# Optimization experiments

Hardware: AMD Instinct MI355X
Metric: run time of the kernel (lower is better)

## Reference

```python
import jax, jax.numpy as jnp
import numpy as np

EPS = 1e-6
NUM_HEADS = 16

def _rmsnorm(h, w):
    hf = h.astype(jnp.float32)
    var = jnp.mean(hf * hf, axis=-1, keepdims=True)
    return (w * (hf * jax.lax.rsqrt(var + EPS))).astype(h.dtype)

def _rotary(t, cos, sin):
    # t: [B,N,H,hd]; cos/sin: [N, hd//2]
    tf = t.astype(jnp.float32)
    tr = tf[..., 0::2]
    ti = tf[..., 1::2]
    c = cos[None, :, None, :]
    s = sin[None, :, None, :]
    out_r = tr * c - ti * s
    out_i = tr * s + ti * c
    out = jnp.stack([out_r, out_i], axis=-1).reshape(t.shape)
    return out.astype(t.dtype)

def setup_inputs() -> dict:
    key = jax.random.key(0)
    ks = jax.random.split(key, 8)
    B, N, C = 2, 2048, 1024
    hd = C // NUM_HEADS
    x = jax.random.normal(ks[0], (B, N, C), jnp.float32)
    qkv_w = jax.random.normal(ks[1], (3 * C, C), jnp.float32) * (C ** -0.5)
    q_norm_w = jnp.ones((hd,), jnp.float32)
    k_norm_w = jnp.ones((hd,), jnp.float32)
    proj_w = jax.random.normal(ks[2], (C, C), jnp.float32) * (C ** -0.5)
    proj_b = jnp.zeros((C,), jnp.float32)
    # rotary freqs_cis = exp(i * theta): unit-magnitude cos/sin
    inv_freq = 1.0 / (10000.0 ** (jnp.arange(0, hd, 2, dtype=jnp.float32) / hd))
    ang = jnp.arange(N, dtype=jnp.float32)[:, None] * inv_freq[None, :]
    pos_cos = jnp.cos(ang)
    pos_sin = jnp.sin(ang)
    mask = jnp.tril(jnp.ones((N, N), dtype=bool))
    return {"x": x, "qkv_w": qkv_w, "q_norm_w": q_norm_w, "k_norm_w": k_norm_w,
            "proj_w": proj_w, "proj_b": proj_b, "pos_cos": pos_cos,
            "pos_sin": pos_sin, "mask": mask}

def reference(x, qkv_w, q_norm_w, k_norm_w, proj_w, proj_b, pos_cos, pos_sin, mask):
    B, N, C = x.shape
    H = NUM_HEADS
    hd = C // H
    qkv = (x @ qkv_w.T).reshape(B, N, 3, H, hd)
    q, k, v = qkv[:, :, 0], qkv[:, :, 1], qkv[:, :, 2]  # [B,N,H,hd]
    q = _rmsnorm(q, q_norm_w)
    k = _rmsnorm(k, k_norm_w)
    q = _rotary(q, pos_cos, pos_sin)
    k = _rotary(k, pos_cos, pos_sin)
    q = q.transpose(0, 2, 1, 3)  # [B,H,N,hd]
    k = k.transpose(0, 2, 1, 3)
    v = v.transpose(0, 2, 1, 3)
    scale = hd ** -0.5
    scores = jnp.einsum('bhqd,bhkd->bhqk', q, k) * scale
    scores = jnp.where(mask[None, None, :, :], scores, jnp.float32(-1e30))
    attn = jax.nn.softmax(scores, axis=-1)
    out = jnp.einsum('bhqk,bhkd->bhqd', attn, v)
    out = out.transpose(0, 2, 1, 3).reshape(B, N, C)
    return out @ proj_w.T + proj_b
```

## Files before the change

kernel.cpp:

```cpp
#include <hip/hip_runtime.h>

using u16 = unsigned short;
using short4v = __attribute__((ext_vector_type(4))) short;
using short8 = __attribute__((ext_vector_type(8))) short;
using floatx4 = __attribute__((ext_vector_type(4))) float;

__device__ __forceinline__ float bf2f(u16 h) {
  union { unsigned int u; float f; } v;
  v.u = ((unsigned int)h) << 16;
  return v.f;
}
__device__ __forceinline__ u16 f2bf(float f) {
  union { float f; unsigned int u; } v;
  v.f = f;
  unsigned int u = v.u;
  return (u16)((u + 0x7FFFu + ((u >> 16) & 1u)) >> 16);
}
__device__ __forceinline__ u16 f2bf_rtz(float f) {
  union { float f; unsigned int u; } v;
  v.f = f;
  return (u16)(v.u >> 16);
}

__device__ __forceinline__ float exp2_raw(float x) {
  return __builtin_amdgcn_exp2f(x);
}
__device__ __forceinline__ float rcp_raw(float x) {
  return __builtin_amdgcn_rcpf(x);
}

typedef const __attribute__((address_space(1))) unsigned int* gas_t;
typedef __attribute__((address_space(3))) unsigned int* las_t;
__device__ __forceinline__ void gl_lds16(const u16* g, u16* l) {
  __builtin_amdgcn_global_load_lds((gas_t)(const void*)g, (las_t)(void*)l, 16,
                                   0, 0);
}

#define MFMA32 __builtin_amdgcn_mfma_f32_16x16x32_bf16

#define QSCALE 0.180336880111f

__global__ __launch_bounds__(256) void cvt_all(
    const float* __restrict__ x, const float* __restrict__ wq,
    const float* __restrict__ wp, u16* __restrict__ xb, u16* __restrict__ wqb,
    u16* __restrict__ wpb) {
#pragma unroll
  for (int j = 0; j < 4; j++) {
    int i = blockIdx.x * 256 + threadIdx.x + j * 524288;
    const float* src;
    u16* dst;
    int off;
    if (i < 1048576) {
      src = x; dst = xb; off = i;
    } else if (i < 1048576 + 786432) {
      src = wq; dst = wqb; off = i - 1048576;
    } else {
      src = wp; dst = wpb; off = i - 1835008;
    }
    float4 v = ((const float4*)src)[off];
    ushort4 o;
    o.x = f2bf(v.x);
    o.y = f2bf(v.y);
    o.z = f2bf(v.z);
    o.w = f2bf(v.w);
    ((ushort4*)dst)[off] = o;
  }
}

template <int BIAS, int OUTBF16, int MT>
__global__ __launch_bounds__(256) void gemm_nt(
    const u16* __restrict__ A, const u16* __restrict__ B,
    const float* __restrict__ bias, void* __restrict__ Cout,
    int M, int N, int K) {
  constexpr int ROWS_A = MT * 32;
  __shared__ u16 As[ROWS_A * 64];
  __shared__ u16 Bs[128 * 64];
  const int tid = threadIdx.x;
  const int lane = tid & 63;
  const int wave = tid >> 6;
  const int col = lane & 15;
  const int quad = lane >> 4;
  const int bm = blockIdx.y * ROWS_A;
  const int bn = blockIdx.x * 128;
  const int wm = (wave >> 1) * (MT * 16);
  const int wn = (wave & 1) * 64;
  const int rsw = col & 7;

  floatx4 acc[MT][4] = {};

  for (int kb = 0; kb < K; kb += 64) {
    __syncthreads();
#pragma unroll
    for (int c = tid; c < ROWS_A * 8; c += 256) {
      const int row = c >> 3, s = (c & 7) ^ (row & 7);
      gl_lds16(A + (size_t)(bm + row) * K + kb + s * 8, As + c * 8);
    }
#pragma unroll
    for (int c = tid; c < 1024; c += 256) {
      const int row = c >> 3, s = (c & 7) ^ (row & 7);
      gl_lds16(B + (size_t)(bn + row) * K + kb + s * 8, Bs + c * 8);
    }
    __syncthreads();

#pragma unroll
    for (int kk = 0; kk < 2; kk++) {
      short8 af[MT], bfr[4];
#pragma unroll
      for (int i = 0; i < MT; i++)
        af[i] = *(const short8*)(As + (wm + i * 16 + col) * 64 +
                                 ((kk * 4 + quad) ^ rsw) * 8);
#pragma unroll
      for (int i = 0; i < 4; i++)
        bfr[i] = *(const short8*)(Bs + (wn + i * 16 + col) * 64 +
                                  ((kk * 4 + quad) ^ rsw) * 8);
#pragma unroll
      for (int mi = 0; mi < MT; mi++)
#pragma unroll
        for (int ni = 0; ni < 4; ni++)
          acc[mi][ni] = MFMA32(af[mi], bfr[ni], acc[mi][ni], 0, 0, 0);
    }
  }

#pragma unroll
  for (int mi = 0; mi < MT; mi++) {
#pragma unroll
    for (int ni = 0; ni < 4; ni++) {
#pragma unroll
      for (int r = 0; r < 4; r++) {
        int row = bm + wm + mi * 16 + quad * 4 + r;
        int c = bn + wn + ni * 16 + col;
        float v = acc[mi][ni][r];
        if (BIAS) v += bias[c];
        if (OUTBF16)
          ((u16*)Cout)[(size_t)row * N + c] = f2bf(v);
        else
          ((float*)Cout)[(size_t)row * N + c] = v;
      }
    }
  }
}

__global__ __launch_bounds__(256) void gemm_qkv(
    const u16* __restrict__ A, const u16* __restrict__ B,
    const float* __restrict__ qw, const float* __restrict__ kw,
    const float* __restrict__ pcos, const float* __restrict__ psin,
    u16* __restrict__ Qb, u16* __restrict__ Kb, u16* __restrict__ Vt) {
  constexpr int K = 1024;
  __shared__ u16 As[128 * 64];
  __shared__ u16 Bs[128 * 64];
  const int tid = threadIdx.x;
  const int lane = tid & 63;
  const int wave = tid >> 6;
  const int col = lane & 15;
  const int quad = lane >> 4;
  const int bm = blockIdx.y * 128;
  const int bn = blockIdx.x * 128;
  const int wm = (wave >> 1) * 64;
  const int wn = (wave & 1) * 64;
  const int rsw = col & 7;

  floatx4 acc[4][4] = {};

  for (int kb = 0; kb < K; kb += 64) {
    __syncthreads();
#pragma unroll
    for (int c = tid; c < 1024; c += 256) {
      const int row = c >> 3, s = (c & 7) ^ (row & 7);
      gl_lds16(A + (size_t)(bm + row) * K + kb + s * 8, As + c * 8);
    }
#pragma unroll
    for (int c = tid; c < 1024; c += 256) {
      const int row = c >> 3, s = (c & 7) ^ (row & 7);
      gl_lds16(B + (size_t)(bn + row) * K + kb + s * 8, Bs + c * 8);
    }
    __syncthreads();

#pragma unroll
    for (int kk = 0; kk < 2; kk++) {
      short8 af[4], bfr[4];
#pragma unroll
      for (int i = 0; i < 4; i++)
        af[i] = *(const short8*)(As + (wm + i * 16 + col) * 64 +
                                 ((kk * 4 + quad) ^ rsw) * 8);
#pragma unroll
      for (int i = 0; i < 4; i++)
        bfr[i] = *(const short8*)(Bs + (wn + i * 16 + col) * 64 +
                                  ((kk * 4 + quad) ^ rsw) * 8);
#pragma unroll
      for (int mi = 0; mi < 4; mi++)
#pragma unroll
        for (int ni = 0; ni < 4; ni++)
          acc[mi][ni] = MFMA32(af[mi], bfr[ni], acc[mi][ni], 0, 0, 0);
    }
  }

  const int c0 = bn + wn;
  const int type = c0 >> 10;
  const int h = (c0 >> 6) & 15;
  const int b = bm >> 11;
  const int bh = b * 16 + h;
  const int nt0 = (bm & 2047) + wm;

  __syncthreads();

  if (type == 2) {
#pragma unroll
    for (int mi = 0; mi < 4; mi++) {
#pragma unroll
      for (int ni = 0; ni < 4; ni++) {
        const int d = ni * 16 + col;
        const int n0 = nt0 + mi * 16 + quad * 4;
        short4v pk;
#pragma unroll
        for (int r = 0; r < 4; r++) pk[r] = (short)f2bf(acc[mi][ni][r]);
        *(short4v*)&Vt[((size_t)(bh * 64 + d)) * 2048 + n0] = pk;
      }
    }
  } else {
    u16* const T = (wave < 2 ? As : Bs) + (wave & 1) * 4096;
    u16* const dst = type ? Kb : Qb;
    const float* const nw = type ? kw : qw;
    float wloc[4];
#pragma unroll
    for (int ni = 0; ni < 4; ni++) wloc[ni] = nw[ni * 16 + col];

#pragma unroll
    for (int mh = 0; mh < 2; mh++) {
#pragma unroll
      for (int mm = 0; mm < 2; mm++) {
        const int mi = mh * 2 + mm;
        floatx4 ss = {};
#pragma unroll
        for (int ni = 0; ni < 4; ni++)
#pragma unroll
          for (int r = 0; r < 4; r++)
            ss[r] += acc[mi][ni][r] * acc[mi][ni][r];
#pragma unroll
        for (int off = 1; off <= 8; off <<= 1)
#pragma unroll
          for (int r = 0; r < 4; r++) ss[r] += __shfl_xor(ss[r], off);
        floatx4 rn;
#pragma unroll
        for (int r = 0; r < 4; r++)
          rn[r] = rsqrtf(ss[r] * (1.0f / 64.0f) + 1e-6f);

#pragma unroll
        for (int ni = 0; ni < 4; ni++) {
          float nv[4], pv[4];
#pragma unroll
          for (int r = 0; r < 4; r++)
            nv[r] = acc[mi][ni][r] * rn[r] * wloc[ni];
#pragma unroll
          for (int r = 0; r < 4; r++) pv[r] = __shfl_xor(nv[r], 1);
#pragma unroll
          for (int r = 0; r < 4; r++) {
            const int n = nt0 + mi * 16 + quad * 4 + r;
            const float cc = pcos[n * 32 + ni * 8 + (col >> 1)];
            const float sn = psin[n * 32 + ni * 8 + (col >> 1)];
            float out = (col & 1) ? pv[r] * sn + nv[r] * cc
                                  : nv[r] * cc - pv[r] * sn;
            if (type == 0) out *= QSCALE;
            T[(mm * 16 + quad * 4 + r) * 80 + ni * 16 + col] = f2bf(out);
          }
        }
      }
      const int tl = lane >> 3;
      const int dc = (lane & 7) * 8;
#pragma unroll
      for (int i = 0; i < 4; i++) {
        short8 v = *(const short8*)&T[(i * 8 + tl) * 80 + dc];
        const int n = nt0 + mh * 32 + i * 8 + tl;
        *(short8*)&dst[((size_t)(bh * 2048 + n)) * 64 + dc] = v;
      }
    }
  }
}

__global__ __launch_bounds__(256) void attn_flash(
    const u16* __restrict__ Q, const u16* __restrict__ Kk,
    const u16* __restrict__ Vt, u16* __restrict__ O) {
  __shared__ u16 Ks[2][2][64 * 32];
  __shared__ u16 Vs[2][2][64 * 32];
  __shared__ u16 Pb[4][16 * 64];
  const int id = blockIdx.x;
  const int bh = id & 31;
  const int tile = 31 - (id >> 5);
  const int tid = threadIdx.x;
  const int lane = tid & 63;
  const int wave = tid >> 6;
  const int col = lane & 15;
  const int quad = lane >> 4;
  const int srow = tid >> 2;
  const int sswz = ((tid & 3) ^ (srow & 3)) * 8;
  const int rq = (quad ^ (col & 3)) * 8;
  const int pswz = (col & 7) << 1;

  const u16* Qh = Q + (size_t)bh * 2048 * 64;
  const u16* Kh = Kk + (size_t)bh * 2048 * 64;
  const u16* Vh = Vt + (size_t)bh * 64 * 2048;
  const int b = bh >> 4, h = bh & 15;

  const int q0 = tile * 64 + wave * 16;

  short8 aq[2];
#pragma unroll
  for (int ks = 0; ks < 2; ks++)
    aq[ks] = *(const short8*)(Qh + (size_t)(q0 + col) * 64 + ks * 32 + quad * 8);

  short8 ones;
#pragma unroll
  for (int j = 0; j < 8; j++) ones[j] = (short)0x3F80;

  floatx4 accO[4] = {};
  floatx4 lacc = {};
  const int nsteps = tile + 1;

#pragma unroll
  for (int half = 0; half < 2; half++) {
    gl_lds16(Kh + (size_t)srow * 64 + half * 32 + sswz,
             &Ks[0][half][0] + tid * 8);
    gl_lds16(Vh + (size_t)srow * 2048 + half * 32 + sswz,
             &Vs[0][half][0] + tid * 8);
  }
  __syncthreads();

  int cur = 0;
  for (int kt = 0; kt < nsteps; kt++) {
    const int j0 = kt * 64;

    if (kt + 1 < nsteps) {
      const int j1 = j0 + 64;
#pragma unroll
      for (int half = 0; half < 2; half++) {
        gl_lds16(Kh + (size_t)(j1 + srow) * 64 + half * 32 + sswz,
                 &Ks[cur ^ 1][half][0] + tid * 8);
        gl_lds16(Vh + (size_t)srow * 2048 + j1 + half * 32 + sswz,
                 &Vs[cur ^ 1][half][0] + tid * 8);
      }
    }

    floatx4 s[4] = {};
#pragma unroll
    for (int nt = 0; nt < 4; nt++) {
#pragma unroll
      for (int ks = 0; ks < 2; ks++) {
        short8 bk = *(const short8*)&Ks[cur][ks][(nt * 16 + col) * 32 + rq];
        s[nt] = MFMA32(bk, aq[ks], s[nt], 0, 0, 0);
      }
    }

    if (j0 + 63 <= q0) {
#pragma unroll
      for (int nt = 0; nt < 4; nt++) {
        short4v pk;
#pragma unroll
        for (int r = 0; r < 4; r++)
          pk[r] = (short)f2bf_rtz(exp2_raw(s[nt][r]));
        *(short4v*)&Pb[wave][col * 64 + ((nt * 4 + quad) ^ pswz) * 4] = pk;
      }
    } else {
      const int qg = q0 + col;
#pragma unroll
      for (int nt = 0; nt < 4; nt++) {
        const int jgb = j0 + nt * 16 + quad * 4;
        short4v pk;
#pragma unroll
        for (int r = 0; r < 4; r++) {
          float pv = (jgb + r <= qg) ? exp2_raw(s[nt][r]) : 0.0f;
          pk[r] = (short)f2bf_rtz(pv);
        }
        *(short4v*)&Pb[wave][col * 64 + ((nt * 4 + quad) ^ pswz) * 4] = pk;
      }
    }

    short8 ap[2];
#pragma unroll
    for (int kf = 0; kf < 2; kf++)
      ap[kf] = *(const short8*)&Pb[wave][col * 64 +
                                         ((kf * 8 + quad * 2) ^ pswz) * 4];

#pragma unroll
    for (int kf = 0; kf < 2; kf++)
      lacc = MFMA32(ap[kf], ones, lacc, 0, 0, 0);

#pragma unroll
    for (int nt = 0; nt < 4; nt++) {
#pragma unroll
      for (int kf = 0; kf < 2; kf++) {
        short8 bv = *(const short8*)&Vs[cur][kf][(nt * 16 + col) * 32 + rq];
        accO[nt] = MFMA32(ap[kf], bv, accO[nt], 0, 0, 0);
      }
    }

    __syncthreads();
    cur ^= 1;
  }

  float lrec[4];
#pragma unroll
  for (int r = 0; r < 4; r++) lrec[r] = rcp_raw(lacc[r]);

#pragma unroll
  for (int nt = 0; nt < 4; nt++) {
#pragma unroll
    for (int r = 0; r < 4; r++) {
      int qg = q0 + quad * 4 + r;
      int d = nt * 16 + col;
      O[((size_t)(b * 2048 + qg) * 16 + h) * 64 + d] =
          f2bf(accO[nt][r] * lrec[r]);
    }
  }
}

extern "C" void kernel_launch(void* const* d_in, const int* in_sizes, int n_in,
                              void* d_out, int out_size, void* d_ws,
                              size_t ws_size, hipStream_t stream) {
  const float* x = (const float*)d_in[0];
  const float* qkv_w = (const float*)d_in[1];
  const float* q_norm_w = (const float*)d_in[2];
  const float* k_norm_w = (const float*)d_in[3];
  const float* proj_w = (const float*)d_in[4];
  const float* proj_b = (const float*)d_in[5];
  const float* pos_cos = (const float*)d_in[6];
  const float* pos_sin = (const float*)d_in[7];

  char* ws = (char*)d_ws;
  u16* xb = (u16*)ws;
  u16* wqkvb = (u16*)(ws + 8388608);
  u16* wprojb = (u16*)(ws + 14680064);
  u16* Qb = (u16*)(ws + 41943040);
  u16* Kb = (u16*)(ws + 50331648);
  u16* Vt = (u16*)(ws + 58720256);
  u16* AO = (u16*)(ws + 67108864);

  cvt_all<<<2048, 256, 0, stream>>>(x, qkv_w, proj_w, xb, wqkvb, wprojb);

  gemm_qkv<<<dim3(24, 32), 256, 0, stream>>>(xb, wqkvb, q_norm_w, k_norm_w,
                                             pos_cos, pos_sin, Qb, Kb, Vt);

  attn_flash<<<dim3(1024), 256, 0, stream>>>(Qb, Kb, Vt, AO);

  gemm_nt<1, 0, 1><<<dim3(8, 128), 256, 0, stream>>>(AO, wprojb, proj_b,
                                                     (float*)d_out, 4096, 1024,
                                                     1024);
}
```

Measured before the change: 197.9 us.

## Process two 16-row query groups per wave in flash attention, halving block size

Each attention block now uses 2 waves instead of 4, and each wave handles 32 query rows as two 16-row groups. Every K and V fragment read from LDS feeds two MFMAs, halving LDS reads per unit of math. Tile loads are split across fewer threads, and register pressure rises from the doubled accumulators. The coarser causal-mask check per wave may also cause slightly more masked work.

```diff
diff --git a/kernel.cpp b/kernel.cpp
--- a/kernel.cpp
+++ b/kernel.cpp
@@ -276,12 +276,12 @@
   }
 }
 
-__global__ __launch_bounds__(256) void attn_flash(
+__global__ __launch_bounds__(128) void attn_flash(
     const u16* __restrict__ Q, const u16* __restrict__ Kk,
     const u16* __restrict__ Vt, u16* __restrict__ O) {
   __shared__ u16 Ks[2][2][64 * 32];
   __shared__ u16 Vs[2][2][64 * 32];
-  __shared__ u16 Pb[4][16 * 64];
+  __shared__ u16 Pb[2][2][16 * 64];
   const int id = blockIdx.x;
   const int bh = id & 31;
   const int tile = 31 - (id >> 5);
@@ -290,8 +290,6 @@
   const int wave = tid >> 6;
   const int col = lane & 15;
   const int quad = lane >> 4;
-  const int srow = tid >> 2;
-  const int sswz = ((tid & 3) ^ (srow & 3)) * 8;
   const int rq = (quad ^ (col & 3)) * 8;
   const int pswz = (col & 7) << 1;
 
@@ -300,27 +298,35 @@
   const u16* Vh = Vt + (size_t)bh * 64 * 2048;
   const int b = bh >> 4, h = bh & 15;
 
-  const int q0 = tile * 64 + wave * 16;
-
-  short8 aq[2];
-#pragma unroll
-  for (int ks = 0; ks < 2; ks++)
-    aq[ks] = *(const short8*)(Qh + (size_t)(q0 + col) * 64 + ks * 32 + quad * 8);
+  const int q0w = tile * 64 + wave * 32;
+  const int nsteps = tile + 1;
+
+  short8 aq[2][2];
+#pragma unroll
+  for (int qg = 0; qg < 2; qg++)
+#pragma unroll
+    for (int ks = 0; ks < 2; ks++)
+      aq[qg][ks] = *(const short8*)(Qh +
+                                    (size_t)(q0w + qg * 16 + col) * 64 +
+                                    ks * 32 + quad * 8);
 
   short8 ones;
 #pragma unroll
   for (int j = 0; j < 8; j++) ones[j] = (short)0x3F80;
 
-  floatx4 accO[4] = {};
-  floatx4 lacc = {};
-  const int nsteps = tile + 1;
+  floatx4 accO[2][4] = {};
+  floatx4 lacc[2] = {};
 
 #pragma unroll
   for (int half = 0; half < 2; half++) {
-    gl_lds16(Kh + (size_t)srow * 64 + half * 32 + sswz,
-             &Ks[0][half][0] + tid * 8);
-    gl_lds16(Vh + (size_t)srow * 2048 + half * 32 + sswz,
-             &Vs[0][half][0] + tid * 8);
+#pragma unroll
+    for (int c = tid; c < 256; c += 128) {
+      const int row = c >> 2, sp = ((c & 3) ^ (row & 3)) * 8;
+      gl_lds16(Kh + (size_t)row * 64 + half * 32 + sp,
+               &Ks[0][half][0] + c * 8);
+      gl_lds16(Vh + (size_t)row * 2048 + half * 32 + sp,
+               &Vs[0][half][0] + c * 8);
+    }
   }
   __syncthreads();
 
@@ -332,63 +338,82 @@
       const int j1 = j0 + 64;
 #pragma unroll
       for (int half = 0; half < 2; half++) {
-        gl_lds16(Kh + (size_t)(j1 + srow) * 64 + half * 32 + sswz,
-                 &Ks[cur ^ 1][half][0] + tid * 8);
-        gl_lds16(Vh + (size_t)srow * 2048 + j1 + half * 32 + sswz,
-                 &Vs[cur ^ 1][half][0] + tid * 8);
-      }
-    }
-
-    floatx4 s[4] = {};
+#pragma unroll
+        for (int c = tid; c < 256; c += 128) {
+          const int row = c >> 2, sp = ((c & 3) ^ (row & 3)) * 8;
+          gl_lds16(Kh + (size_t)(j1 + row) * 64 + half * 32 + sp,
+                   &Ks[cur ^ 1][half][0] + c * 8);
+          gl_lds16(Vh + (size_t)row * 2048 + j1 + half * 32 + sp,
+                   &Vs[cur ^ 1][half][0] + c * 8);
+        }
+      }
+    }
+
+    floatx4 s[2][4] = {};
 #pragma unroll
     for (int nt = 0; nt < 4; nt++) {
 #pragma unroll
       for (int ks = 0; ks < 2; ks++) {
         short8 bk = *(const short8*)&Ks[cur][ks][(nt * 16 + col) * 32 + rq];
-        s[nt] = MFMA32(bk, aq[ks], s[nt], 0, 0, 0);
-      }
-    }
-
-    if (j0 + 63 <= q0) {
-#pragma unroll
-      for (int nt = 0; nt < 4; nt++) {
-        short4v pk;
-#pragma unroll
-        for (int r = 0; r < 4; r++)
-          pk[r] = (short)f2bf_rtz(exp2_raw(s[nt][r]));
-        *(short4v*)&Pb[wave][col * 64 + ((nt * 4 + quad) ^ pswz) * 4] = pk;
-      }
+#pragma unroll
+        for (int qg = 0; qg < 2; qg++)
+          s[qg][nt] = MFMA32(bk, aq[qg][ks], s[qg][nt], 0, 0, 0);
+      }
+    }
+
+    if (j0 + 63 <= q0w) {
+#pragma unroll
+      for (int qg = 0; qg < 2; qg++)
+#pragma unroll
+        for (int nt = 0; nt < 4; nt++) {
+          short4v pk;
+#pragma unroll
+          for (int r = 0; r < 4; r++)
+            pk[r] = (short)f2bf_rtz(exp2_raw(s[qg][nt][r]));
+          *(short4v*)&Pb[wave][qg][col * 64 + ((nt * 4 + quad) ^ pswz) * 4] =
+              pk;
+        }
     } else {
-      const int qg = q0 + col;
-#pragma unroll
-      for (int nt = 0; nt < 4; nt++) {
-        const int jgb = j0 + nt * 16 + quad * 4;
-        short4v pk;
-#pragma unroll
-        for (int r = 0; r < 4; r++) {
-          float pv = (jgb + r <= qg) ? exp2_raw(s[nt][r]) : 0.0f;
-          pk[r] = (short)f2bf_rtz(pv);
+#pragma unroll
+      for (int qg = 0; qg < 2; qg++) {
+        const int qq = q0w + qg * 16 + col;
+#pragma unroll
+        for (int nt = 0; nt < 4; nt++) {
+          const int jgb = j0 + nt * 16 + quad * 4;
+          short4v pk;
+#pragma unroll
+          for (int r = 0; r < 4; r++) {
+            float pv = (jgb + r <= qq) ? exp2_raw(s[qg][nt][r]) : 0.0f;
+            pk[r] = (short)f2bf_rtz(pv);
+          }
+          *(short4v*)&Pb[wave][qg][col * 64 + ((nt * 4 + quad) ^ pswz) * 4] =
+              pk;
         }
-        *(short4v*)&Pb[wave][col * 64 + ((nt * 4 + quad) ^ pswz) * 4] = pk;
-      }
-    }
-
-    short8 ap[2];
-#pragma unroll
-    for (int kf = 0; kf < 2; kf++)
-      ap[kf] = *(const short8*)&Pb[wave][col * 64 +
-                                         ((kf * 8 + quad * 2) ^ pswz) * 4];
-
-#pragma unroll
-    for (int kf = 0; kf < 2; kf++)
-      lacc = MFMA32(ap[kf], ones, lacc, 0, 0, 0);
+      }
+    }
+
+    short8 ap[2][2];
+#pragma unroll
+    for (int qg = 0; qg < 2; qg++)
+#pragma unroll
+      for (int kf = 0; kf < 2; kf++)
+        ap[qg][kf] = *(const short8*)&Pb[wave][qg]
+                         [col * 64 + ((kf * 8 + quad * 2) ^ pswz) * 4];
+
+#pragma unroll
+    for (int qg = 0; qg < 2; qg++)
+#pragma unroll
+      for (int kf = 0; kf < 2; kf++)
+        lacc[qg] = MFMA32(ap[qg][kf], ones, lacc[qg], 0, 0, 0);
 
 #pragma unroll
     for (int nt = 0; nt < 4; nt++) {
 #pragma unroll
       for (int kf = 0; kf < 2; kf++) {
         short8 bv = *(const short8*)&Vs[cur][kf][(nt * 16 + col) * 32 + rq];
-        accO[nt] = MFMA32(ap[kf], bv, accO[nt], 0, 0, 0);
+#pragma unroll
+        for (int qg = 0; qg < 2; qg++)
+          accO[qg][nt] = MFMA32(ap[qg][kf], bv, accO[qg][nt], 0, 0, 0);
       }
     }
 
@@ -396,18 +421,20 @@
     cur ^= 1;
   }
 
-  float lrec[4];
-#pragma unroll
-  for (int r = 0; r < 4; r++) lrec[r] = rcp_raw(lacc[r]);
-
-#pragma unroll
-  for (int nt = 0; nt < 4; nt++) {
-#pragma unroll
-    for (int r = 0; r < 4; r++) {
-      int qg = q0 + quad * 4 + r;
-      int d = nt * 16 + col;
-      O[((size_t)(b * 2048 + qg) * 16 + h) * 64 + d] =
-          f2bf(accO[nt][r] * lrec[r]);
+#pragma unroll
+  for (int qg = 0; qg < 2; qg++) {
+    floatx4 lr;
+#pragma unroll
+    for (int r = 0; r < 4; r++) lr[r] = rcp_raw(lacc[qg][r]);
+#pragma unroll
+    for (int nt = 0; nt < 4; nt++) {
+#pragma unroll
+      for (int r = 0; r < 4; r++) {
+        const int qq = q0w + qg * 16 + quad * 4 + r;
+        const int d = nt * 16 + col;
+        O[((size_t)(b * 2048 + qq) * 16 + h) * 64 + d] =
+            f2bf(accO[qg][nt][r] * lr[r]);
+      }
     }
   }
 }
@@ -438,7 +465,7 @@
   gemm_qkv<<<dim3(24, 32), 256, 0, stream>>>(xb, wqkvb, q_norm_w, k_norm_w,
                                              pos_cos, pos_sin, Qb, Kb, Vt);
 
-  attn_flash<<<dim3(1024), 256, 0, stream>>>(Qb, Kb, Vt, AO);
+  attn_flash<<<dim3(1024), 128, 0, stream>>>(Qb, Kb, Vt, AO);
 
   gemm_nt<1, 0, 1><<<dim3(8, 128), 256, 0, stream>>>(AO, wprojb, proj_b,
                                                      (float*)d_out, 4096, 1024,
```

Result: slower. 203.7 us (+2.9%).
